# Kernel optimization log

Hardware: AMD Instinct MI355X
Metric: run time of the kernel (lower is better)

Reference implementation:

```python
import jax, jax.numpy as jnp
import numpy as np

N_NODES = 370
N_EEG = 64
HID = 64
L = 8
KS = 2
EMB = 16
KTOP = N_NODES // 10  # 37, as in the torch code


def _gcn_norm_dense(A):
    # A[dst, src] dense adjacency. torch_geometric GCNConv gcn_norm:
    # add self-loop weight 1.0 only for nodes lacking one, then D^-1/2 A D^-1/2.
    d0 = jnp.diagonal(A)
    A = A + jnp.diag(jnp.where(d0 > 0, 0.0, 1.0))
    deg = A.sum(axis=1)  # weighted in-degree at dst (incl. self loops)
    dinv = jnp.where(deg > 0, jax.lax.rsqrt(deg), 0.0)
    return dinv[:, None] * A * dinv[None, :]


def _adaptive_adj(emb_src, emb_tgt):
    # softmax(relu(S T^T)) row-wise, keep top-k per row (softmax vals are all >0)
    adj = jax.nn.softmax(jax.nn.relu(emb_src @ emb_tgt.T), axis=-1)
    vals, idx = jax.lax.top_k(adj, KTOP)
    sp = jnp.zeros_like(adj).at[jnp.arange(adj.shape[0])[:, None], idx].set(vals)
    return _gcn_norm_dense(sp)


def _causal_conv(h, w, b, dilation):
    # h: (BN, H, T), w: (H_out, H_in, K); left-pad by (K-1)*dilation => causal
    pad = (w.shape[-1] - 1) * dilation
    out = jax.lax.conv_general_dilated(
        h, w, window_strides=(1,), padding=[(pad, 0)],
        rhs_dilation=(dilation,), dimension_numbers=("NCH", "OIH", "NCH"))
    return out + b[None, :, None]


def _layernorm(x, g, b, eps=1e-5):
    m = x.mean(-1, keepdims=True)
    v = ((x - m) ** 2).mean(-1, keepdims=True)
    return (x - m) * jax.lax.rsqrt(v + eps) * g + b


def _gelu(x):
    return jax.nn.gelu(x, approximate=False)


def setup_inputs() -> dict:
    key = jax.random.key(0)
    ks = iter(jax.random.split(key, 64))
    B, T, E = 8, 64, 7400

    x = jax.random.normal(next(ks), (B, T, N_NODES, HID), jnp.float32)
    src = jax.random.randint(next(ks), (E,), 0, N_NODES, jnp.int32)
    off = jax.random.randint(next(ks), (E,), 1, N_NODES, jnp.int32)
    edge_index = jnp.stack([src, (src + off) % N_NODES])  # self-loop free
    edge_weight = jax.random.uniform(next(ks), (E,), jnp.float32)

    def rn(shape, scale):
        return jax.random.normal(next(ks), shape, jnp.float32) * scale

    s = 1.0 / np.sqrt(HID)
    inp = {
        "x": x, "edge_index": edge_index, "edge_weight": edge_weight,
        "in_W": rn((HID, HID), s), "in_b": rn((HID,), 0.01),
        "gcnf_W": rn((L, HID, HID), s), "gcnf_b": rn((L, HID), 0.01),
        "emb_src": rn((L, N_NODES, EMB), 1.0),  # torch.randn init
        "emb_tgt": rn((L, N_NODES, EMB), 1.0),
        "gcna_W": rn((L, HID, HID), s), "gcna_b": rn((L, HID), 0.01),
        "filt_W": rn((L, HID, HID, KS), s), "filt_b": rn((L, HID), 0.01),
        "gate_W": rn((L, HID, HID, KS), s), "gate_b": rn((L, HID), 0.01),
        "res_W": rn((L, HID, HID), s), "res_b": rn((L, HID), 0.01),
        "skip_W": rn((L, HID, HID), s), "skip_b": rn((L, HID), 0.01),
        "ln_g": jnp.ones((L, HID), jnp.float32), "ln_b": jnp.zeros((L, HID), jnp.float32),
        "end1_W": rn((HID, HID), s), "end1_b": rn((HID,), 0.01),
        "end2_W": rn((HID, HID), s), "end2_b": rn((HID,), 0.01),
        "eeg1_W": rn((N_NODES * HID, 256), 1.0 / np.sqrt(N_NODES * HID)), "eeg1_b": rn((256,), 0.01),
        "eeg2_W": rn((256, N_EEG), 1.0 / 16.0), "eeg2_b": rn((N_EEG,), 0.01),
    }
    return inp


def reference(x, edge_index, edge_weight, in_W, in_b, gcnf_W, gcnf_b,
              emb_src, emb_tgt, gcna_W, gcna_b, filt_W, filt_b, gate_W, gate_b,
              res_W, res_b, skip_W, skip_b, ln_g, ln_b,
              end1_W, end1_b, end2_W, end2_b, eeg1_W, eeg1_b, eeg2_W, eeg2_b):
    B, T, N, H = x.shape
    x = x @ in_W + in_b  # input_proj

    # Fixed (DTI prior) adjacency: same for every layer, build & normalize once.
    A = jnp.zeros((N, N), x.dtype).at[edge_index[1], edge_index[0]].add(edge_weight)
    A = _gcn_norm_dense(A)

    skip_sum = jnp.zeros_like(x)
    for i in range(L):  # fixed small layer count
        dil = 2 ** (i % 4)
        xf = x.reshape(B * T, N, H)
        h_fixed = jnp.einsum("mn,bnh->bmh", A, xf @ gcnf_W[i]) + gcnf_b[i]
        Aa = _adaptive_adj(emb_src[i], emb_tgt[i])
        h_adapt = jnp.einsum("mn,bnh->bmh", Aa, xf @ gcna_W[i]) + gcna_b[i]
        h = (h_fixed + h_adapt).reshape(B, T, N, H)
        h = h.transpose(0, 2, 3, 1).reshape(B * N, H, T)
        h = jnp.tanh(_causal_conv(h, filt_W[i], filt_b[i], dil)) * \
            jax.nn.sigmoid(_causal_conv(h, gate_W[i], gate_b[i], dil))
        # 1x1 convs over channel dim (dropout is identity in eval)
        skip = (jnp.einsum("oi,nit->not", skip_W[i], h) + skip_b[i][None, :, None])
        res = (jnp.einsum("oi,nit->not", res_W[i], h) + res_b[i][None, :, None])
        skip = skip.reshape(B, N, H, T).transpose(0, 3, 1, 2)
        res = res.reshape(B, N, H, T).transpose(0, 3, 1, 2)
        x = _layernorm(res + x, ln_g[i], ln_b[i])
        skip_sum = skip_sum + skip

    h = _gelu(skip_sum) @ end1_W + end1_b
    h = _gelu(h) @ end2_W + end2_b
    h = h.reshape(B, T, N * H)  # GraphToEEG
    h = _gelu(h @ eeg1_W + eeg1_b) @ eeg2_W + eeg2_b
    return h
```

## Files before the change

kernel.cpp:

```cpp
#include <hip/hip_runtime.h>
#include <hip/hip_bf16.h>
#include <math.h>

typedef __attribute__((ext_vector_type(8))) short bf16x8;
typedef __attribute__((ext_vector_type(4))) float f32x4;
typedef unsigned short u16;
typedef unsigned int u32;
typedef unsigned long long u64;

#define NN 370
#define HH 64
#define LL 8
#define TT 64
#define BTOT 512
#define RR (BTOT*NN)
#define KTOPK 37
#define SPLITK 37

__device__ inline u16 f2bf(float f){
  __hip_bfloat16 h = __float2bfloat16(f);
  return __builtin_bit_cast(u16, h);
}
__device__ inline float bf2f(short s){
  u32 v = ((u32)(u16)s) << 16;
  return __builtin_bit_cast(float, v);
}
__device__ inline float gelu_f(float x){ return 0.5f * x * (1.0f + erff(x * 0.70710678118654752440f)); }

__device__ inline void sts16(char* lds, int row, int kb, int stride, bf16x8 v){
  *reinterpret_cast<bf16x8*>(lds + row*stride + (kb ^ ((row&7)<<4))) = v;
}
__device__ inline bf16x8 lds16(const char* lds, int row, int kb, int stride){
  return *reinterpret_cast<const bf16x8*>(lds + row*stride + (kb ^ ((row&7)<<4)));
}
__device__ inline bf16x8 gldB(const char* Bt, int c, int kb, int stride){
  return *reinterpret_cast<const bf16x8*>(Bt + c*stride + (kb ^ ((c&7)<<4)));
}
__device__ inline void copyB(char* dst, const u16* src, int bytes, int tid, int nthr){
  for(int o = tid*16; o < bytes; o += nthr*16)
    *reinterpret_cast<bf16x8*>(dst + o) =
      *reinterpret_cast<const bf16x8*>(reinterpret_cast<const char*>(src) + o);
}

template<int NT, int KT>
__device__ inline void mma_core(const char* sA, const char* sB, int strideA, int strideB,
                                f32x4* acc, int ln, int mt){
#pragma unroll
  for(int nt=0; nt<NT; ++nt) acc[nt] = f32x4{0.f,0.f,0.f,0.f};
#pragma unroll
  for(int kt=0; kt<KT; ++kt){
    int kb = kt*64 + ((ln>>4)<<4);
    bf16x8 a = lds16(sA, mt*16 + (ln&15), kb, strideA);
#pragma unroll
    for(int nt=0; nt<NT; ++nt){
      bf16x8 b = lds16(sB, nt*16 + (ln&15), kb, strideB);
      acc[nt] = __builtin_amdgcn_mfma_f32_16x16x32_bf16(a, b, acc[nt], 0, 0, 0);
    }
  }
}

__global__ void kzero(float* __restrict__ p, size_t n){
  for(size_t i = (size_t)blockIdx.x*256 + threadIdx.x; i < n; i += (size_t)gridDim.x*256) p[i] = 0.f;
}

__global__ void kbuildA(const int* __restrict__ ei, const float* __restrict__ ew, float* __restrict__ Araw, int E){
  int e = blockIdx.x*256 + threadIdx.x;
  if(e < E){
    int src = ei[e], dst = ei[E + e];
    atomicAdd(&Araw[dst*NN + src], ew[e]);
  }
}

__global__ __launch_bounds__(384) void knormF(float* __restrict__ Araw, float* __restrict__ dinvF){
  int i = threadIdx.x;
  if(i < NN){
    float d0 = Araw[i*NN+i];
    if(d0 == 0.f) Araw[i*NN+i] = 1.f;
    float s = 0.f;
    for(int j=0;j<NN;++j) s += Araw[i*NN+j];
    dinvF[i] = rsqrtf(s);
  }
}

__global__ __launch_bounds__(512) void kadapt(const float* __restrict__ esrc, const float* __restrict__ etgt,
                                              float* __restrict__ ArawA, float* __restrict__ dinvA){
  __shared__ float tgT[16][372];
  __shared__ float red[8];
  __shared__ u64 keys[512];
  __shared__ int diagflag;
  int i = blockIdx.x, l = blockIdx.y, tid = threadIdx.x;
  const float* Et = etgt + (size_t)l*NN*16;
  for(int idx = tid; idx < NN*16; idx += 512)
    tgT[idx & 15][idx >> 4] = Et[idx];
  float sr[16];
  const float* Es = esrc + ((size_t)l*NN + i)*16;
#pragma unroll
  for(int k=0;k<16;k++) sr[k] = Es[k];
  if(tid == 0) diagflag = 0;
  __syncthreads();
  bool act = tid < NN;
  float s = 0.f;
  if(act){
    float d = 0.f;
#pragma unroll
    for(int k=0;k<16;k++) d += sr[k]*tgT[k][tid];
    s = fmaxf(d, 0.f);
  }
  float v = act ? s : -1.f;
#pragma unroll
  for(int o=1;o<64;o<<=1) v = fmaxf(v, __shfl_xor(v,o,64));
  if((tid&63)==0) red[tid>>6] = v;
  __syncthreads();
  float mx = red[0];
#pragma unroll
  for(int q=1;q<8;q++) mx = fmaxf(mx, red[q]);
  __syncthreads();
  float e = act ? expf(s - mx) : 0.f;
  float t = e;
#pragma unroll
  for(int o=1;o<64;o<<=1) t += __shfl_xor(t,o,64);
  if((tid&63)==0) red[tid>>6] = t;
  __syncthreads();
  float sum = 0.f;
#pragma unroll
  for(int q=0;q<8;q++) sum += red[q];
  float p = e / sum;
  u32 fb = __builtin_bit_cast(u32, p);
  keys[tid] = act ? ((((u64)fb)<<32) | (u64)(0xFFFFFFFFu - (u32)tid)) : 0ULL;
  __syncthreads();
  for(int k2=2; k2<=512; k2<<=1){
    for(int j=k2>>1; j>0; j>>=1){
      int ixj = tid ^ j;
      if(ixj > tid){
        u64 a = keys[tid], b = keys[ixj];
        bool dirUp = ((tid & k2) == 0);
        if(dirUp ? (a < b) : (a > b)){ keys[tid] = b; keys[ixj] = a; }
      }
      __syncthreads();
    }
  }
  float myval = 0.f; int myidx = -1;
  if(tid < KTOPK){
    u64 kk = keys[tid];
    myidx = (int)(0xFFFFFFFFu - (u32)kk);
    myval = __builtin_bit_cast(float, (u32)(kk>>32));
    if(myidx == i) diagflag = 1;
  }
  __syncthreads();
  float dsum = (tid < KTOPK) ? myval : 0.f;
  if(tid < 64){
#pragma unroll
    for(int o=1;o<64;o<<=1) dsum += __shfl_xor(dsum,o,64);
    if(tid == 0) dinvA[l*NN + i] = rsqrtf(dsum + (diagflag ? 0.f : 1.f));
  }
  if(tid < KTOPK) ArawA[((size_t)l*NN + i)*NN + myidx] = myval;
  if(tid == 0 && !diagflag) ArawA[((size_t)l*NN + i)*NN + i] = 1.f;
}

__global__ void kacat(const float* __restrict__ Araw, const float* __restrict__ ArawA,
                      const float* __restrict__ dinvF, const float* __restrict__ dinvA,
                      u16* __restrict__ Acat){
  int idx = blockIdx.x*256 + threadIdx.x;
  if(idx >= LL*384*768) return;
  int k = idx % 768; int m = (idx / 768) % 384; int l = idx / (768*384);
  float v = 0.f;
  if(m < NN){
    if(k < 384){
      if(k < NN) v = dinvF[m]*Araw[m*NN+k]*dinvF[k];
    } else {
      int n = k - 384;
      if(n < NN) v = dinvA[l*NN+m]*ArawA[((size_t)l*NN+m)*NN+n]*dinvA[l*NN+n];
    }
  }
  Acat[idx] = f2bf(v);
}

__global__ void kbt_small(const float* __restrict__ inW, const float* __restrict__ e1W, const float* __restrict__ e2W,
                          u16* __restrict__ BtIN, u16* __restrict__ BtE1, u16* __restrict__ BtE2){
  const float* W = blockIdx.x==0 ? inW : (blockIdx.x==1 ? e1W : e2W);
  u16* Bt = blockIdx.x==0 ? BtIN : (blockIdx.x==1 ? BtE1 : BtE2);
  for(int idx = threadIdx.x; idx < 4096; idx += 256){
    int c = idx >> 6, k = idx & 63;
    *(u16*)((char*)Bt + c*128 + ((k*2) ^ ((c&7)<<4))) = f2bf(W[k*64 + c]);
  }
}

__global__ void kbt_layer(const float* __restrict__ gcnfW, const float* __restrict__ gcnaW,
                          const float* __restrict__ filtW, const float* __restrict__ gateW,
                          const float* __restrict__ skipW, const float* __restrict__ resW,
                          u16* __restrict__ BtUV, u16* __restrict__ BtCV, u16* __restrict__ BtSR){
  int l = blockIdx.x, which = blockIdx.y;
  if(which == 0){
    u16* Bt = BtUV + (size_t)l*128*64;
    for(int idx=threadIdx.x; idx<8192; idx+=256){
      int c = idx>>6, k = idx&63;
      float v = (c<64) ? gcnfW[(size_t)l*4096 + k*64 + c] : gcnaW[(size_t)l*4096 + k*64 + (c-64)];
      *(u16*)((char*)Bt + c*128 + ((k*2) ^ ((c&7)<<4))) = f2bf(v);
    }
  } else if(which == 1){
    u16* Bt = BtCV + (size_t)l*128*128;
    for(int idx=threadIdx.x; idx<16384; idx+=256){
      int c = idx>>7, k = idx&127;
      const float* W = (c<64) ? filtW : gateW;
      int o = c & 63, ii = k & 63, tap = (k<64) ? 1 : 0;
      float v = W[(size_t)l*8192 + o*128 + ii*2 + tap];
      *(u16*)((char*)Bt + c*256 + ((k*2) ^ ((c&7)<<4))) = f2bf(v);
    }
  } else {
    u16* Bt = BtSR + (size_t)l*128*64;
    for(int idx=threadIdx.x; idx<8192; idx+=256){
      int c = idx>>6, k = idx&63;
      float v = (c<64) ? skipW[(size_t)l*4096 + c*64 + k] : resW[(size_t)l*4096 + (c-64)*64 + k];
      *(u16*)((char*)Bt + c*128 + ((k*2) ^ ((c&7)<<4))) = f2bf(v);
    }
  }
}

__global__ void ktrans(const float* __restrict__ W, u16* __restrict__ Wt){
  __shared__ float tile[64][65];
  int kb = blockIdx.x*64, cb = blockIdx.y*64;
  for(int idx = threadIdx.x; idx < 4096; idx += 256){
    int kk = idx>>6, cc = idx&63;
    tile[kk][cc] = W[(size_t)(kb+kk)*256 + cb+cc];
  }
  __syncthreads();
  for(int idx = threadIdx.x; idx < 4096; idx += 256){
    int cc = idx>>6, kk = idx&63;
    Wt[(size_t)(cb+cc)*23680 + kb+kk] = f2bf(tile[kk][cc]);
  }
}

__global__ __launch_bounds__(256) void krowmm_in(const float* __restrict__ X, const u16* __restrict__ Bt,
                                                 const float* __restrict__ bias,
                                                 u16* __restrict__ xbf){
  int tid = threadIdx.x;
  int w = tid>>6, ln = tid&63, lr = ln&15, hi = ln>>4;
  int kboff = hi<<4;
  size_t r = (size_t)blockIdx.x*64 + w*16 + lr;
  f32x4 acc[4];
#pragma unroll
  for(int i=0;i<4;i++) acc[i] = f32x4{0.f,0.f,0.f,0.f};
  const char* BI = (const char*)Bt;
#pragma unroll
  for(int kt=0; kt<2; ++kt){
    const float* xr = X + r*64 + kt*32 + hi*8;
    float4 pa = ((const float4*)xr)[0], pb = ((const float4*)xr)[1];
    bf16x8 a;
    a[0]=(short)f2bf(pa.x); a[1]=(short)f2bf(pa.y); a[2]=(short)f2bf(pa.z); a[3]=(short)f2bf(pa.w);
    a[4]=(short)f2bf(pb.x); a[5]=(short)f2bf(pb.y); a[6]=(short)f2bf(pb.z); a[7]=(short)f2bf(pb.w);
#pragma unroll
    for(int nt=0; nt<4; ++nt){
      bf16x8 b = gldB(BI, nt*16 + lr, kt*64 + kboff, 128);
      acc[nt] = __builtin_amdgcn_mfma_f32_16x16x32_bf16(a, b, acc[nt], 0, 0, 0);
    }
  }
  size_t r0 = (size_t)blockIdx.x*64;
#pragma unroll
  for(int nt=0; nt<4; ++nt){
    int c = nt*16 + lr;
    float bv = bias[c];
#pragma unroll
    for(int rr=0;rr<4;++rr){
      int row = w*16 + hi*4 + rr;
      xbf[(r0+row)*64 + c] = f2bf(acc[nt][rr] + bv);
    }
  }
}

__global__ __launch_bounds__(512) void kgcn(const u16* __restrict__ xbf, const u16* __restrict__ BtUV,
                                            const u16* __restrict__ Acat,
                                            const float* __restrict__ bfb, const float* __restrict__ bab,
                                            u16* __restrict__ t2){
  __shared__ char uvt[64*768];
  int bt = blockIdx.x, tid = threadIdx.x;
  int w = tid>>6, ln = tid&63, lr = ln&15, hi = ln>>4;
  int kboff = hi<<4;
  f32x4 acc[12];
#pragma unroll
  for(int j=0;j<12;j++) acc[j] = f32x4{0.f,0.f,0.f,0.f};
  const char* xb = (const char*)(xbf + (size_t)bt*NN*64);
  for(int p=0; p<2; ++p){
    bf16x8 bw[2][4];
#pragma unroll
    for(int kt=0;kt<2;++kt)
#pragma unroll
      for(int nt=0;nt<4;++nt){
        int c = p*64 + nt*16 + lr;
        bw[kt][nt] = *reinterpret_cast<const bf16x8*>((const char*)BtUV + c*128 + ((kt*64 + kboff) ^ ((c&7)<<4)));
      }
    f32x4 uvacc[3][4];
#pragma unroll
    for(int mi=0;mi<3;++mi)
#pragma unroll
      for(int nt=0;nt<4;++nt) uvacc[mi][nt] = f32x4{0.f,0.f,0.f,0.f};
#pragma unroll
    for(int mi=0;mi<3;++mi){
      int node = (w*3+mi)*16 + lr;
#pragma unroll
      for(int kt=0;kt<2;++kt){
        bf16x8 a;
        if(node < NN) a = *reinterpret_cast<const bf16x8*>(xb + (size_t)node*128 + kt*64 + kboff);
        else { bf16x8 z = {0,0,0,0,0,0,0,0}; a = z; }
#pragma unroll
        for(int nt=0;nt<4;++nt)
          uvacc[mi][nt] = __builtin_amdgcn_mfma_f32_16x16x32_bf16(a, bw[kt][nt], uvacc[mi][nt], 0,0,0);
      }
    }
    __syncthreads();
#pragma unroll
    for(int mi=0;mi<3;++mi){
      int nd = (w*3+mi)*16 + hi*4;
#pragma unroll
      for(int nt=0;nt<4;++nt){
        int cl = nt*16 + lr;
        u64 pk = (u64)((u32)f2bf(uvacc[mi][nt][0]) | ((u32)f2bf(uvacc[mi][nt][1])<<16))
               | ((u64)((u32)f2bf(uvacc[mi][nt][2]) | ((u32)f2bf(uvacc[mi][nt][3])<<16)) << 32);
        *(u64*)(uvt + cl*768 + ((nd*2) ^ ((cl&7)<<4))) = pk;
      }
    }
    __syncthreads();
    const char* abase = (const char*)Acat + p*768 + kboff;
#pragma unroll
    for(int kt=0; kt<12; ++kt){
      bf16x8 a0 = *reinterpret_cast<const bf16x8*>(abase + (size_t)((w*3+0)*16 + lr)*1536 + kt*64);
      bf16x8 a1 = *reinterpret_cast<const bf16x8*>(abase + (size_t)((w*3+1)*16 + lr)*1536 + kt*64);
      bf16x8 a2 = *reinterpret_cast<const bf16x8*>(abase + (size_t)((w*3+2)*16 + lr)*1536 + kt*64);
      bf16x8 b0 = lds16(uvt, 0*16 + lr, kt*64 + kboff, 768);
      bf16x8 b1 = lds16(uvt, 1*16 + lr, kt*64 + kboff, 768);
      bf16x8 b2 = lds16(uvt, 2*16 + lr, kt*64 + kboff, 768);
      bf16x8 b3 = lds16(uvt, 3*16 + lr, kt*64 + kboff, 768);
      acc[0]  = __builtin_amdgcn_mfma_f32_16x16x32_bf16(a0, b0, acc[0],  0,0,0);
      acc[1]  = __builtin_amdgcn_mfma_f32_16x16x32_bf16(a0, b1, acc[1],  0,0,0);
      acc[2]  = __builtin_amdgcn_mfma_f32_16x16x32_bf16(a0, b2, acc[2],  0,0,0);
      acc[3]  = __builtin_amdgcn_mfma_f32_16x16x32_bf16(a0, b3, acc[3],  0,0,0);
      acc[4]  = __builtin_amdgcn_mfma_f32_16x16x32_bf16(a1, b0, acc[4],  0,0,0);
      acc[5]  = __builtin_amdgcn_mfma_f32_16x16x32_bf16(a1, b1, acc[5],  0,0,0);
      acc[6]  = __builtin_amdgcn_mfma_f32_16x16x32_bf16(a1, b2, acc[6],  0,0,0);
      acc[7]  = __builtin_amdgcn_mfma_f32_16x16x32_bf16(a1, b3, acc[7],  0,0,0);
      acc[8]  = __builtin_amdgcn_mfma_f32_16x16x32_bf16(a2, b0, acc[8],  0,0,0);
      acc[9]  = __builtin_amdgcn_mfma_f32_16x16x32_bf16(a2, b1, acc[9],  0,0,0);
      acc[10] = __builtin_amdgcn_mfma_f32_16x16x32_bf16(a2, b2, acc[10], 0,0,0);
      acc[11] = __builtin_amdgcn_mfma_f32_16x16x32_bf16(a2, b3, acc[11], 0,0,0);
    }
  }
#pragma unroll
  for(int mi=0; mi<3; ++mi){
    int mt = w*3 + mi;
    int mbase = mt*16 + hi*4;
#pragma unroll
    for(int nt=0; nt<4; ++nt){
      int col = nt*16 + lr;
      float bias = bfb[col] + bab[col];
#pragma unroll
      for(int r=0;r<4;++r){
        int m = mbase + r;
        if(m < NN) t2[((size_t)bt*NN + m)*64 + col] = f2bf(acc[mi*4+nt][r] + bias);
      }
    }
  }
}

__global__ __launch_bounds__(256) void kcsr(const u16* __restrict__ t2, const u16* __restrict__ BtC,
                                            const u16* __restrict__ BtS,
                                            const float* __restrict__ fb, const float* __restrict__ gb,
                                            const float* __restrict__ sb, const float* __restrict__ rb,
                                            const float* __restrict__ lng, const float* __restrict__ lnb,
                                            u16* __restrict__ skip,
                                            u16* __restrict__ xbf, int dil, int first, int douv){
  __shared__ char sA[64*128];
  int blk = blockIdx.x, tid = threadIdx.x;
  int w = tid>>6, ln = tid&63, lr = ln&15, hi = ln>>4;
  int kboff = hi<<4;
  int r0 = blk*64;
  int r = r0 + w*16 + lr;
  int t = (r / NN) & (TT-1);
  const char* cur = (const char*)t2 + (size_t)r*128;
  const char* prv = cur - (size_t)dil*NN*128;
  bf16x8 a0 = *reinterpret_cast<const bf16x8*>(cur + kboff);
  bf16x8 a1 = *reinterpret_cast<const bf16x8*>(cur + 64 + kboff);
  bf16x8 a2, a3;
  if(t >= dil){
    a2 = *reinterpret_cast<const bf16x8*>(prv + kboff);
    a3 = *reinterpret_cast<const bf16x8*>(prv + 64 + kboff);
  } else {
    bf16x8 z = {0,0,0,0,0,0,0,0}; a2 = z; a3 = z;
  }
  const char* BC = (const char*)BtC;
  f32x4 acc[8];
#pragma unroll
  for(int i=0;i<8;i++) acc[i] = f32x4{0.f,0.f,0.f,0.f};
  bf16x8 afr[4] = {a0, a1, a2, a3};
#pragma unroll
  for(int kt=0; kt<4; ++kt){
    bf16x8 bfr[8];
#pragma unroll
    for(int nt=0; nt<8; ++nt)
      bfr[nt] = gldB(BC, nt*16 + lr, kt*64 + kboff, 256);
#pragma unroll
    for(int nt=0; nt<8; ++nt)
      acc[nt] = __builtin_amdgcn_mfma_f32_16x16x32_bf16(afr[kt], bfr[nt], acc[nt], 0, 0, 0);
  }
  u16 q[4][4];
#pragma unroll
  for(int nt=0; nt<4; ++nt){
    int o = nt*16 + lr;
    float fbv = fb[o], gbv = gb[o];
#pragma unroll
    for(int rr=0;rr<4;++rr){
      float fv = acc[nt][rr] + fbv;
      float gv = acc[nt+4][rr] + gbv;
      float ef = __expf(-2.f*fv);
      float th = (1.f - ef) / (1.f + ef);
      float sg = 1.f / (1.f + __expf(-gv));
      q[nt][rr] = f2bf(th * sg);
    }
  }
#pragma unroll
  for(int nt=0; nt<4; ++nt){
    int col = nt*16 + lr;
#pragma unroll
    for(int rr=0;rr<4;++rr){
      int row = w*16 + hi*4 + rr;
      *(u16*)(sA + row*128 + ((col*2) ^ ((row&7)<<4))) = q[nt][rr];
    }
  }
  __syncthreads();
  const char* BS = (const char*)BtS;
  f32x4 as[8];
#pragma unroll
  for(int i=0;i<8;i++) as[i] = f32x4{0.f,0.f,0.f,0.f};
#pragma unroll
  for(int kt=0; kt<2; ++kt){
    bf16x8 a = lds16(sA, w*16 + lr, kt*64 + kboff, 128);
    bf16x8 bfr[8];
#pragma unroll
    for(int nt=0; nt<8; ++nt)
      bfr[nt] = gldB(BS, nt*16 + lr, kt*64 + kboff, 128);
#pragma unroll
    for(int nt=0; nt<8; ++nt)
      as[nt] = __builtin_amdgcn_mfma_f32_16x16x32_bf16(a, bfr[nt], as[nt], 0, 0, 0);
  }
  size_t g0 = (size_t)r0;
  f32x4 y[4];
  f32x4 sum = {0.f,0.f,0.f,0.f}, ssq = {0.f,0.f,0.f,0.f};
#pragma unroll
  for(int nt=0; nt<4; ++nt){
    int col = nt*16 + lr;
    float rbv = rb[col];
#pragma unroll
    for(int rr=0;rr<4;++rr){
      int row = w*16 + hi*4 + rr;
      float xo = bf2f((short)xbf[(g0+row)*64 + col]);
      float vv = as[4+nt][rr] + rbv + xo;
      y[nt][rr] = vv; sum[rr] += vv; ssq[rr] += vv*vv;
    }
  }
#pragma unroll
  for(int o=1;o<16;o<<=1){
#pragma unroll
    for(int rr=0;rr<4;++rr){
      sum[rr] += __shfl_xor(sum[rr], o, 64);
      ssq[rr] += __shfl_xor(ssq[rr], o, 64);
    }
  }
  f32x4 mval, rstd;
#pragma unroll
  for(int rr=0;rr<4;++rr){
    float m = sum[rr] * (1.f/64.f);
    float var = ssq[rr] * (1.f/64.f) - m*m;
    mval[rr] = m; rstd[rr] = rsqrtf(var + 1e-5f);
  }
#pragma unroll
  for(int nt=0; nt<4; ++nt){
    int col = nt*16 + lr;
    float g = lng[col], bb = lnb[col], sbv = sb[col];
#pragma unroll
    for(int rr=0;rr<4;++rr){
      int row = w*16 + hi*4 + rr;
      size_t gi = (g0+row)*64 + col;
      float xo = (y[nt][rr] - mval[rr]) * rstd[rr] * g + bb;
      if(douv) xbf[gi] = f2bf(xo);
      float s = as[nt][rr] + sbv;
      if(first) skip[gi] = f2bf(s);
      else      skip[gi] = f2bf(bf2f((short)skip[gi]) + s);
    }
  }
}

__global__ __launch_bounds__(256) void kend2(const u16* __restrict__ skip, const u16* __restrict__ Bt1,
                                             const u16* __restrict__ Bt2, const float* __restrict__ b1,
                                             const float* __restrict__ b2, u16* __restrict__ h2){
  __shared__ char sA[8192];
  int tid = threadIdx.x;
  int w = tid>>6, ln = tid&63, lr = ln&15, hi = ln>>4;
  int kboff = hi<<4;
  size_t r = (size_t)blockIdx.x*64 + w*16 + lr;
  const char* B1 = (const char*)Bt1;
  const char* B2 = (const char*)Bt2;
  f32x4 acc[4];
#pragma unroll
  for(int i=0;i<4;i++) acc[i] = f32x4{0.f,0.f,0.f,0.f};
#pragma unroll
  for(int kt=0; kt<2; ++kt){
    bf16x8 a = *reinterpret_cast<const bf16x8*>((const char*)skip + r*128 + kt*64 + kboff);
#pragma unroll
    for(int i=0;i<8;i++) a[i] = (short)f2bf(gelu_f(bf2f(a[i])));
#pragma unroll
    for(int nt=0; nt<4; ++nt){
      bf16x8 b = gldB(B1, nt*16 + lr, kt*64 + kboff, 128);
      acc[nt] = __builtin_amdgcn_mfma_f32_16x16x32_bf16(a, b, acc[nt], 0, 0, 0);
    }
  }
  u16 xq[4][4];
#pragma unroll
  for(int nt=0; nt<4; ++nt){
    int c = nt*16 + lr;
    float bv = b1[c];
#pragma unroll
    for(int rr=0;rr<4;++rr) xq[nt][rr] = f2bf(gelu_f(acc[nt][rr] + bv));
  }
#pragma unroll
  for(int nt=0; nt<4; ++nt){
    int col = nt*16 + lr;
#pragma unroll
    for(int rr=0;rr<4;++rr){
      int row = w*16 + hi*4 + rr;
      *(u16*)(sA + row*128 + ((col*2) ^ ((row&7)<<4))) = xq[nt][rr];
    }
  }
  __syncthreads();
  f32x4 a2[4];
#pragma unroll
  for(int i=0;i<4;i++) a2[i] = f32x4{0.f,0.f,0.f,0.f};
#pragma unroll
  for(int kt=0; kt<2; ++kt){
    bf16x8 a = lds16(sA, w*16 + lr, kt*64 + kboff, 128);
#pragma unroll
    for(int nt=0; nt<4; ++nt){
      bf16x8 b = gldB(B2, nt*16 + lr, kt*64 + kboff, 128);
      a2[nt] = __builtin_amdgcn_mfma_f32_16x16x32_bf16(a, b, a2[nt], 0, 0, 0);
    }
  }
  size_t rbase = (size_t)blockIdx.x*64 + w*16 + hi*4;
#pragma unroll
  for(int nt=0; nt<4; ++nt){
    int c = nt*16 + lr;
    float bv = b2[c];
#pragma unroll
    for(int rr=0;rr<4;++rr) h2[(rbase+rr)*64 + c] = f2bf(a2[nt][rr] + bv);
  }
}

__global__ __launch_bounds__(512) void keeg1(const u16* __restrict__ h2, const u16* __restrict__ WtE,
                                             float* __restrict__ part){
  __shared__ char sA[64*128];
  __shared__ char sB[256*128];
  int rowg = blockIdx.x, sp = blockIdx.y;
  int tid = threadIdx.x, w = tid>>6, ln = tid&63;
  f32x4 acc[8];
#pragma unroll
  for(int i=0;i<8;i++) acc[i] = f32x4{0.f,0.f,0.f,0.f};
  int mt = w & 3, ntb = (w>>2)*8;
  for(int ks=0; ks<20; ++ks){
    int k0 = (sp*20 + ks)*32;
    __syncthreads();
    for(int s = tid; s < 256; s += 512){
      int row = s>>2, kc = s&3;
      bf16x8 v = *reinterpret_cast<const bf16x8*>(h2 + (size_t)(rowg*64+row)*23680 + k0 + kc*8);
      sts16(sA, row, kc*16, 128, v);
    }
    for(int s = tid; s < 1024; s += 512){
      int row = s>>2, kc = s&3;
      bf16x8 v = *reinterpret_cast<const bf16x8*>(WtE + (size_t)row*23680 + k0 + kc*8);
      sts16(sB, row, kc*16, 128, v);
    }
    __syncthreads();
    bf16x8 a = lds16(sA, mt*16 + (ln&15), ((ln>>4)<<4), 128);
#pragma unroll
    for(int j=0;j<8;++j){
      bf16x8 b = lds16(sB, (ntb+j)*16 + (ln&15), ((ln>>4)<<4), 128);
      acc[j] = __builtin_amdgcn_mfma_f32_16x16x32_bf16(a, b, acc[j], 0, 0, 0);
    }
  }
  float* dst = part + ((size_t)sp*512 + rowg*64)*256;
#pragma unroll
  for(int j=0;j<8;++j){
    int c = (ntb+j)*16 + (ln&15);
#pragma unroll
    for(int r=0;r<4;++r){
      int row = mt*16 + ((ln>>4)<<2) + r;
      dst[(size_t)row*256 + c] = acc[j][r];
    }
  }
}

__global__ __launch_bounds__(256) void keeg2(const float* __restrict__ part, const float* __restrict__ b1,
                                             const float* __restrict__ W2, const float* __restrict__ b2,
                                             float* __restrict__ out){
  __shared__ float u[256];
  __shared__ float pr[4][64];
  int bt = blockIdx.x, tid = threadIdx.x;
  float sacc = 0.f;
  for(int sp2=0; sp2<SPLITK; ++sp2) sacc += part[((size_t)sp2*512 + bt)*256 + tid];
  u[tid] = gelu_f(sacc + b1[tid]);
  __syncthreads();
  int w = tid>>6, ln = tid&63;
  float acc = 0.f;
  for(int c = w*64; c < (w+1)*64; ++c) acc += u[c] * W2[c*64 + ln];
  pr[w][ln] = acc;
  __syncthreads();
  if(tid < 64)
    out[(size_t)bt*64 + tid] = pr[0][tid]+pr[1][tid]+pr[2][tid]+pr[3][tid] + b2[tid];
}

extern "C" void kernel_launch(void* const* d_in, const int* in_sizes, int n_in,
                              void* d_out, int out_size, void* d_ws, size_t ws_size,
                              hipStream_t stream){
  const float* x_in  = (const float*)d_in[0];
  const int*   ei    = (const int*)d_in[1];
  const float* ew    = (const float*)d_in[2];
  const float* in_W  = (const float*)d_in[3];
  const float* in_b  = (const float*)d_in[4];
  const float* gcnfW = (const float*)d_in[5];
  const float* gcnfb = (const float*)d_in[6];
  const float* esrc  = (const float*)d_in[7];
  const float* etgt  = (const float*)d_in[8];
  const float* gcnaW = (const float*)d_in[9];
  const float* gcnab = (const float*)d_in[10];
  const float* filtW = (const float*)d_in[11];
  const float* filtb = (const float*)d_in[12];
  const float* gateW = (const float*)d_in[13];
  const float* gateb = (const float*)d_in[14];
  const float* resW  = (const float*)d_in[15];
  const float* resb  = (const float*)d_in[16];
  const float* skipW = (const float*)d_in[17];
  const float* skipb = (const float*)d_in[18];
  const float* lng   = (const float*)d_in[19];
  const float* lnb   = (const float*)d_in[20];
  const float* e1W   = (const float*)d_in[21];
  const float* e1b   = (const float*)d_in[22];
  const float* e2W   = (const float*)d_in[23];
  const float* e2b   = (const float*)d_in[24];
  const float* eg1W  = (const float*)d_in[25];
  const float* eg1b  = (const float*)d_in[26];
  const float* eg2W  = (const float*)d_in[27];
  const float* eg2b  = (const float*)d_in[28];
  int E = in_sizes[2];

  char* p = (char*)d_ws;
  auto carve = [&](size_t bytes)->char*{ char* r = p; p += (bytes + 255) & ~(size_t)255; return r; };
  u16*   xbf   = (u16*)  carve((size_t)RR*64*2);
  u16*   skip  = (u16*)  carve((size_t)RR*64*2);
  u16*   t2    = (u16*)  carve((size_t)RR*64*2);
  u16*   h2    = (u16*)  carve((size_t)RR*64*2);
  float* Araw9 = (float*)carve((size_t)9*NN*NN*4);
  float* Araw  = Araw9;
  float* ArawA = Araw9 + (size_t)NN*NN;
  float* dinvF = (float*)carve(NN*4);
  float* dinvA = (float*)carve(LL*NN*4);
  u16*   Acat  = (u16*)  carve((size_t)LL*384*768*2);
  u16*   BtUV  = (u16*)  carve((size_t)LL*128*64*2);
  u16*   BtCV  = (u16*)  carve((size_t)LL*128*128*2);
  u16*   BtSR  = (u16*)  carve((size_t)LL*128*64*2);
  u16*   BtIN  = (u16*)  carve(64*64*2);
  u16*   BtE1  = (u16*)  carve(64*64*2);
  u16*   BtE2  = (u16*)  carve(64*64*2);
  u16*   WtE   = (u16*)  carve((size_t)256*23680*2);
  float* part  = (float*)carve((size_t)SPLITK*512*256*4);

  kzero<<<1024, 256, 0, stream>>>(Araw9, (size_t)9*NN*NN);
  kbuildA<<<(E+255)/256, 256, 0, stream>>>(ei, ew, Araw, E);
  knormF<<<1, 384, 0, stream>>>(Araw, dinvF);
  kadapt<<<dim3(NN, LL), 512, 0, stream>>>(esrc, etgt, ArawA, dinvA);
  kacat<<<(LL*384*768 + 255)/256, 256, 0, stream>>>(Araw, ArawA, dinvF, dinvA, Acat);
  kbt_small<<<3, 256, 0, stream>>>(in_W, e1W, e2W, BtIN, BtE1, BtE2);
  kbt_layer<<<dim3(LL, 3), 256, 0, stream>>>(gcnfW, gcnaW, filtW, gateW, skipW, resW, BtUV, BtCV, BtSR);
  ktrans<<<dim3(370, 4), 256, 0, stream>>>(eg1W, WtE);

  krowmm_in<<<RR/64, 256, 0, stream>>>(x_in, BtIN, in_b, xbf);

  for(int l=0; l<LL; ++l){
    int dil = 1 << (l & 3);
    kgcn<<<BTOT, 512, 0, stream>>>(xbf, BtUV + (size_t)l*8192, Acat + (size_t)l*384*768,
                                   gcnfb + l*64, gcnab + l*64, t2);
    int douv = (l < LL-1) ? 1 : 0;
    kcsr<<<RR/64, 256, 0, stream>>>(t2, BtCV + (size_t)l*16384, BtSR + (size_t)l*8192,
                                    filtb + l*64, gateb + l*64, skipb + l*64, resb + l*64,
                                    lng + l*64, lnb + l*64, skip, xbf, dil, l==0 ? 1 : 0, douv);
  }

  kend2<<<RR/64, 256, 0, stream>>>(skip, BtE1, BtE2, e1b, e2b, h2);
  keeg1<<<dim3(8, SPLITK), 512, 0, stream>>>(h2, WtE, part);
  keeg2<<<BTOT, 256, 0, stream>>>(part, eg1b, eg2W, eg2b, (float*)d_out);
}
```

Before: 1.036 ms.

## Process two graph samples per GCN block and stage kcsr epilogue through LDS

The GCN kernel now runs 1024 threads per block and handles two batch-time samples per block. The node dimension is split into thirds so the shared tile shrinks to 16KB per sample, which is meant to raise occupancy and let the two samples share the cached adjacency reads. The kcsr epilogue now writes the accumulators to a 32KB LDS buffer and re-reads them row-wise, so the LayerNorm, xbf and skip loads and stores become 16-byte vectorised accesses instead of scattered 2-byte ones. In exchange there are more barriers in kgcn (six phases) and extra LDS traffic plus a larger LDS footprint in kcsr, which may limit its occupancy.

```diff
diff --git a/kernel.cpp b/kernel.cpp
--- a/kernel.cpp
+++ b/kernel.cpp
@@ -267,85 +267,80 @@
   }
 }
 
-__global__ __launch_bounds__(512) void kgcn(const u16* __restrict__ xbf, const u16* __restrict__ BtUV,
-                                            const u16* __restrict__ Acat,
-                                            const float* __restrict__ bfb, const float* __restrict__ bab,
-                                            u16* __restrict__ t2){
-  __shared__ char uvt[64*768];
-  int bt = blockIdx.x, tid = threadIdx.x;
+__global__ __launch_bounds__(1024) void kgcn(const u16* __restrict__ xbf, const u16* __restrict__ BtUV,
+                                             const u16* __restrict__ Acat,
+                                             const float* __restrict__ bfb, const float* __restrict__ bab,
+                                             u16* __restrict__ t2){
+  __shared__ char uvt[2*16384];
+  int bt2 = blockIdx.x, tid = threadIdx.x;
   int w = tid>>6, ln = tid&63, lr = ln&15, hi = ln>>4;
   int kboff = hi<<4;
+  int q = w>>3, wq = w&7;
+  int bt = bt2*2 + q;
+  const char* xb = (const char*)(xbf + (size_t)bt*NN*64);
+  char* uq = uvt + q*16384;
   f32x4 acc[12];
 #pragma unroll
   for(int j=0;j<12;j++) acc[j] = f32x4{0.f,0.f,0.f,0.f};
-  const char* xb = (const char*)(xbf + (size_t)bt*NN*64);
-  for(int p=0; p<2; ++p){
-    bf16x8 bw[2][4];
-#pragma unroll
-    for(int kt=0;kt<2;++kt)
-#pragma unroll
-      for(int nt=0;nt<4;++nt){
-        int c = p*64 + nt*16 + lr;
-        bw[kt][nt] = *reinterpret_cast<const bf16x8*>((const char*)BtUV + c*128 + ((kt*64 + kboff) ^ ((c&7)<<4)));
-      }
-    f32x4 uvacc[3][4];
-#pragma unroll
-    for(int mi=0;mi<3;++mi)
-#pragma unroll
-      for(int nt=0;nt<4;++nt) uvacc[mi][nt] = f32x4{0.f,0.f,0.f,0.f};
-#pragma unroll
-    for(int mi=0;mi<3;++mi){
-      int node = (w*3+mi)*16 + lr;
-#pragma unroll
-      for(int kt=0;kt<2;++kt){
-        bf16x8 a;
-        if(node < NN) a = *reinterpret_cast<const bf16x8*>(xb + (size_t)node*128 + kt*64 + kboff);
-        else { bf16x8 z = {0,0,0,0,0,0,0,0}; a = z; }
-#pragma unroll
-        for(int nt=0;nt<4;++nt)
-          uvacc[mi][nt] = __builtin_amdgcn_mfma_f32_16x16x32_bf16(a, bw[kt][nt], uvacc[mi][nt], 0,0,0);
-      }
+#pragma unroll
+  for(int sp=0; sp<6; ++sp){
+    int p = sp/3, third = sp - p*3;
+    int nl = third*128 + wq*16 + lr;
+    bf16x8 a0, a1;
+    if(nl < NN){
+      a0 = *reinterpret_cast<const bf16x8*>(xb + (size_t)nl*128 + kboff);
+      a1 = *reinterpret_cast<const bf16x8*>(xb + (size_t)nl*128 + 64 + kboff);
+    } else {
+      bf16x8 z = {0,0,0,0,0,0,0,0}; a0 = z; a1 = z;
+    }
+    f32x4 uv[4];
+#pragma unroll
+    for(int nt=0;nt<4;++nt) uv[nt] = f32x4{0.f,0.f,0.f,0.f};
+#pragma unroll
+    for(int nt=0;nt<4;++nt){
+      int c = p*64 + nt*16 + lr;
+      bf16x8 b0 = gldB((const char*)BtUV, c, kboff, 128);
+      bf16x8 b1 = gldB((const char*)BtUV, c, 64 + kboff, 128);
+      uv[nt] = __builtin_amdgcn_mfma_f32_16x16x32_bf16(a0, b0, uv[nt], 0,0,0);
+      uv[nt] = __builtin_amdgcn_mfma_f32_16x16x32_bf16(a1, b1, uv[nt], 0,0,0);
     }
     __syncthreads();
-#pragma unroll
-    for(int mi=0;mi<3;++mi){
-      int nd = (w*3+mi)*16 + hi*4;
-#pragma unroll
-      for(int nt=0;nt<4;++nt){
-        int cl = nt*16 + lr;
-        u64 pk = (u64)((u32)f2bf(uvacc[mi][nt][0]) | ((u32)f2bf(uvacc[mi][nt][1])<<16))
-               | ((u64)((u32)f2bf(uvacc[mi][nt][2]) | ((u32)f2bf(uvacc[mi][nt][3])<<16)) << 32);
-        *(u64*)(uvt + cl*768 + ((nd*2) ^ ((cl&7)<<4))) = pk;
-      }
+    int ndl = wq*16 + hi*4;
+#pragma unroll
+    for(int nt=0;nt<4;++nt){
+      int cl = nt*16 + lr;
+      u64 pk = (u64)((u32)f2bf(uv[nt][0]) | ((u32)f2bf(uv[nt][1])<<16))
+             | ((u64)((u32)f2bf(uv[nt][2]) | ((u32)f2bf(uv[nt][3])<<16)) << 32);
+      *(u64*)(uq + cl*256 + ((ndl*2) ^ ((cl&7)<<4))) = pk;
     }
     __syncthreads();
-    const char* abase = (const char*)Acat + p*768 + kboff;
-#pragma unroll
-    for(int kt=0; kt<12; ++kt){
-      bf16x8 a0 = *reinterpret_cast<const bf16x8*>(abase + (size_t)((w*3+0)*16 + lr)*1536 + kt*64);
-      bf16x8 a1 = *reinterpret_cast<const bf16x8*>(abase + (size_t)((w*3+1)*16 + lr)*1536 + kt*64);
-      bf16x8 a2 = *reinterpret_cast<const bf16x8*>(abase + (size_t)((w*3+2)*16 + lr)*1536 + kt*64);
-      bf16x8 b0 = lds16(uvt, 0*16 + lr, kt*64 + kboff, 768);
-      bf16x8 b1 = lds16(uvt, 1*16 + lr, kt*64 + kboff, 768);
-      bf16x8 b2 = lds16(uvt, 2*16 + lr, kt*64 + kboff, 768);
-      bf16x8 b3 = lds16(uvt, 3*16 + lr, kt*64 + kboff, 768);
-      acc[0]  = __builtin_amdgcn_mfma_f32_16x16x32_bf16(a0, b0, acc[0],  0,0,0);
-      acc[1]  = __builtin_amdgcn_mfma_f32_16x16x32_bf16(a0, b1, acc[1],  0,0,0);
-      acc[2]  = __builtin_amdgcn_mfma_f32_16x16x32_bf16(a0, b2, acc[2],  0,0,0);
-      acc[3]  = __builtin_amdgcn_mfma_f32_16x16x32_bf16(a0, b3, acc[3],  0,0,0);
-      acc[4]  = __builtin_amdgcn_mfma_f32_16x16x32_bf16(a1, b0, acc[4],  0,0,0);
-      acc[5]  = __builtin_amdgcn_mfma_f32_16x16x32_bf16(a1, b1, acc[5],  0,0,0);
-      acc[6]  = __builtin_amdgcn_mfma_f32_16x16x32_bf16(a1, b2, acc[6],  0,0,0);
-      acc[7]  = __builtin_amdgcn_mfma_f32_16x16x32_bf16(a1, b3, acc[7],  0,0,0);
-      acc[8]  = __builtin_amdgcn_mfma_f32_16x16x32_bf16(a2, b0, acc[8],  0,0,0);
-      acc[9]  = __builtin_amdgcn_mfma_f32_16x16x32_bf16(a2, b1, acc[9],  0,0,0);
-      acc[10] = __builtin_amdgcn_mfma_f32_16x16x32_bf16(a2, b2, acc[10], 0,0,0);
-      acc[11] = __builtin_amdgcn_mfma_f32_16x16x32_bf16(a2, b3, acc[11], 0,0,0);
+    const char* abase = (const char*)Acat + p*768 + third*256 + kboff;
+#pragma unroll
+    for(int kt=0; kt<4; ++kt){
+      bf16x8 a_0 = *reinterpret_cast<const bf16x8*>(abase + (size_t)((wq*3+0)*16 + lr)*1536 + kt*64);
+      bf16x8 a_1 = *reinterpret_cast<const bf16x8*>(abase + (size_t)((wq*3+1)*16 + lr)*1536 + kt*64);
+      bf16x8 a_2 = *reinterpret_cast<const bf16x8*>(abase + (size_t)((wq*3+2)*16 + lr)*1536 + kt*64);
+      bf16x8 b0 = lds16(uq, 0*16 + lr, kt*64 + kboff, 256);
+      bf16x8 b1 = lds16(uq, 1*16 + lr, kt*64 + kboff, 256);
+      bf16x8 b2 = lds16(uq, 2*16 + lr, kt*64 + kboff, 256);
+      bf16x8 b3 = lds16(uq, 3*16 + lr, kt*64 + kboff, 256);
+      acc[0]  = __builtin_amdgcn_mfma_f32_16x16x32_bf16(a_0, b0, acc[0],  0,0,0);
+      acc[1]  = __builtin_amdgcn_mfma_f32_16x16x32_bf16(a_0, b1, acc[1],  0,0,0);
+      acc[2]  = __builtin_amdgcn_mfma_f32_16x16x32_bf16(a_0, b2, acc[2],  0,0,0);
+      acc[3]  = __builtin_amdgcn_mfma_f32_16x16x32_bf16(a_0, b3, acc[3],  0,0,0);
+      acc[4]  = __builtin_amdgcn_mfma_f32_16x16x32_bf16(a_1, b0, acc[4],  0,0,0);
+      acc[5]  = __builtin_amdgcn_mfma_f32_16x16x32_bf16(a_1, b1, acc[5],  0,0,0);
+      acc[6]  = __builtin_amdgcn_mfma_f32_16x16x32_bf16(a_1, b2, acc[6],  0,0,0);
+      acc[7]  = __builtin_amdgcn_mfma_f32_16x16x32_bf16(a_1, b3, acc[7],  0,0,0);
+      acc[8]  = __builtin_amdgcn_mfma_f32_16x16x32_bf16(a_2, b0, acc[8],  0,0,0);
+      acc[9]  = __builtin_amdgcn_mfma_f32_16x16x32_bf16(a_2, b1, acc[9],  0,0,0);
+      acc[10] = __builtin_amdgcn_mfma_f32_16x16x32_bf16(a_2, b2, acc[10], 0,0,0);
+      acc[11] = __builtin_amdgcn_mfma_f32_16x16x32_bf16(a_2, b3, acc[11], 0,0,0);
     }
   }
 #pragma unroll
   for(int mi=0; mi<3; ++mi){
-    int mt = w*3 + mi;
+    int mt = wq*3 + mi;
     int mbase = mt*16 + hi*4;
 #pragma unroll
     for(int nt=0; nt<4; ++nt){
@@ -367,7 +362,7 @@
                                             const float* __restrict__ lng, const float* __restrict__ lnb,
                                             u16* __restrict__ skip,
                                             u16* __restrict__ xbf, int dil, int first, int douv){
-  __shared__ char sA[64*128];
+  __shared__ char sA[32768];
   int blk = blockIdx.x, tid = threadIdx.x;
   int w = tid>>6, ln = tid&63, lr = ln&15, hi = ln>>4;
   int kboff = hi<<4;
@@ -400,7 +395,7 @@
     for(int nt=0; nt<8; ++nt)
       acc[nt] = __builtin_amdgcn_mfma_f32_16x16x32_bf16(afr[kt], bfr[nt], acc[nt], 0, 0, 0);
   }
-  u16 q[4][4];
+  u16 qv[4][4];
 #pragma unroll
   for(int nt=0; nt<4; ++nt){
     int o = nt*16 + lr;
@@ -412,7 +407,7 @@
       float ef = __expf(-2.f*fv);
       float th = (1.f - ef) / (1.f + ef);
       float sg = 1.f / (1.f + __expf(-gv));
-      q[nt][rr] = f2bf(th * sg);
+      qv[nt][rr] = f2bf(th * sg);
     }
   }
 #pragma unroll
@@ -421,7 +416,7 @@
 #pragma unroll
     for(int rr=0;rr<4;++rr){
       int row = w*16 + hi*4 + rr;
-      *(u16*)(sA + row*128 + ((col*2) ^ ((row&7)<<4))) = q[nt][rr];
+      *(u16*)(sA + row*128 + ((col*2) ^ ((row&7)<<4))) = qv[nt][rr];
     }
   }
   __syncthreads();
@@ -440,51 +435,72 @@
     for(int nt=0; nt<8; ++nt)
       as[nt] = __builtin_amdgcn_mfma_f32_16x16x32_bf16(a, bfr[nt], as[nt], 0, 0, 0);
   }
-  size_t g0 = (size_t)r0;
-  f32x4 y[4];
-  f32x4 sum = {0.f,0.f,0.f,0.f}, ssq = {0.f,0.f,0.f,0.f};
+  __syncthreads();
 #pragma unroll
   for(int nt=0; nt<4; ++nt){
-    int col = nt*16 + lr;
-    float rbv = rb[col];
+    int c = nt*16 + lr;
 #pragma unroll
     for(int rr=0;rr<4;++rr){
       int row = w*16 + hi*4 + rr;
-      float xo = bf2f((short)xbf[(g0+row)*64 + col]);
-      float vv = as[4+nt][rr] + rbv + xo;
-      y[nt][rr] = vv; sum[rr] += vv; ssq[rr] += vv*vv;
-    }
-  }
-#pragma unroll
-  for(int o=1;o<16;o<<=1){
-#pragma unroll
-    for(int rr=0;rr<4;++rr){
-      sum[rr] += __shfl_xor(sum[rr], o, 64);
-      ssq[rr] += __shfl_xor(ssq[rr], o, 64);
-    }
-  }
-  f32x4 mval, rstd;
-#pragma unroll
-  for(int rr=0;rr<4;++rr){
-    float m = sum[rr] * (1.f/64.f);
-    float var = ssq[rr] * (1.f/64.f) - m*m;
-    mval[rr] = m; rstd[rr] = rsqrtf(var + 1e-5f);
-  }
-#pragma unroll
-  for(int nt=0; nt<4; ++nt){
-    int col = nt*16 + lr;
-    float g = lng[col], bb = lnb[col], sbv = sb[col];
-#pragma unroll
-    for(int rr=0;rr<4;++rr){
-      int row = w*16 + hi*4 + rr;
-      size_t gi = (g0+row)*64 + col;
-      float xo = (y[nt][rr] - mval[rr]) * rstd[rr] * g + bb;
-      if(douv) xbf[gi] = f2bf(xo);
-      float s = as[nt][rr] + sbv;
-      if(first) skip[gi] = f2bf(s);
-      else      skip[gi] = f2bf(bf2f((short)skip[gi]) + s);
-    }
-  }
+      *(float*)(sA + row*512 + (((c)*4)      ^ ((row&7)<<4))) = as[nt][rr];
+      *(float*)(sA + row*512 + (((64+c)*4)   ^ ((row&7)<<4))) = as[4+nt][rr];
+    }
+  }
+  __syncthreads();
+  int row = tid >> 2, seg = tid & 3;
+  int c0 = seg * 16;
+  float sk[16], re[16];
+#pragma unroll
+  for(int j=0;j<4;++j){
+    f32x4 vs = *reinterpret_cast<const f32x4*>(sA + row*512 + (((c0 + j*4)*4)      ^ ((row&7)<<4)));
+    f32x4 vr = *reinterpret_cast<const f32x4*>(sA + row*512 + (((64 + c0 + j*4)*4) ^ ((row&7)<<4)));
+#pragma unroll
+    for(int i=0;i<4;++i){ sk[j*4+i] = vs[i]; re[j*4+i] = vr[i]; }
+  }
+  size_t gr = (size_t)(r0 + row)*64 + c0;
+  bf16x8 xv0 = *reinterpret_cast<const bf16x8*>(xbf + gr);
+  bf16x8 xv1 = *reinterpret_cast<const bf16x8*>(xbf + gr + 8);
+  float y[16]; float s1 = 0.f, s2 = 0.f;
+#pragma unroll
+  for(int i=0;i<16;++i){
+    float xo = bf2f(i < 8 ? xv0[i] : xv1[i-8]);
+    float vv = re[i] + rb[c0+i] + xo;
+    y[i] = vv; s1 += vv; s2 += vv*vv;
+  }
+  s1 += __shfl_xor(s1, 1, 64); s1 += __shfl_xor(s1, 2, 64);
+  s2 += __shfl_xor(s2, 1, 64); s2 += __shfl_xor(s2, 2, 64);
+  float m = s1 * (1.f/64.f);
+  float var = s2 * (1.f/64.f) - m*m;
+  float rstd = rsqrtf(var + 1e-5f);
+  if(douv){
+    bf16x8 o0, o1;
+#pragma unroll
+    for(int i=0;i<16;++i){
+      float xo = (y[i] - m) * rstd * lng[c0+i] + lnb[c0+i];
+      if(i < 8) o0[i] = (short)f2bf(xo); else o1[i-8] = (short)f2bf(xo);
+    }
+    *reinterpret_cast<bf16x8*>(xbf + gr) = o0;
+    *reinterpret_cast<bf16x8*>(xbf + gr + 8) = o1;
+  }
+  bf16x8 so0, so1;
+  if(first){
+#pragma unroll
+    for(int i=0;i<16;++i){
+      float sv = sk[i] + sb[c0+i];
+      if(i < 8) so0[i] = (short)f2bf(sv); else so1[i-8] = (short)f2bf(sv);
+    }
+  } else {
+    bf16x8 sp0 = *reinterpret_cast<const bf16x8*>(skip + gr);
+    bf16x8 sp1 = *reinterpret_cast<const bf16x8*>(skip + gr + 8);
+#pragma unroll
+    for(int i=0;i<16;++i){
+      float old = bf2f(i < 8 ? sp0[i] : sp1[i-8]);
+      float sv = old + sk[i] + sb[c0+i];
+      if(i < 8) so0[i] = (short)f2bf(sv); else so1[i-8] = (short)f2bf(sv);
+    }
+  }
+  *reinterpret_cast<bf16x8*>(skip + gr) = so0;
+  *reinterpret_cast<bf16x8*>(skip + gr + 8) = so1;
 }
 
 __global__ __launch_bounds__(256) void kend2(const u16* __restrict__ skip, const u16* __restrict__ Bt1,
@@ -681,8 +697,8 @@
 
   for(int l=0; l<LL; ++l){
     int dil = 1 << (l & 3);
-    kgcn<<<BTOT, 512, 0, stream>>>(xbf, BtUV + (size_t)l*8192, Acat + (size_t)l*384*768,
-                                   gcnfb + l*64, gcnab + l*64, t2);
+    kgcn<<<BTOT/2, 1024, 0, stream>>>(xbf, BtUV + (size_t)l*8192, Acat + (size_t)l*384*768,
+                                      gcnfb + l*64, gcnab + l*64, t2);
     int douv = (l < LL-1) ? 1 : 0;
     kcsr<<<RR/64, 256, 0, stream>>>(t2, BtCV + (size_t)l*16384, BtSR + (size_t)l*8192,
                                     filtb + l*64, gateb + l*64, skipb + l*64, resb + l*64,
```

New measurement: 1.019 ms. No clear change (-1.6%).
